# Optimization experiments

Hardware: AMD Instinct MI355X
Metric: run time of the kernel (lower is better)

## Reference

```python
import jax, jax.numpy as jnp
import numpy as np

N_NODES, N_EDGES, N_RELS, D_IN, D_OUT = 50000, 200000, 64, 32, 32


def setup_inputs() -> dict:
    key = jax.random.key(0)
    k1, k2, k3, k4, k5 = jax.random.split(key, 5)
    feat = jax.random.normal(k1, (N_NODES, D_IN), dtype=jnp.float32)
    # learned per-relation projection weights: [R, D_IN, D_OUT]
    weight = jax.random.normal(k2, (N_RELS, D_IN, D_OUT), dtype=jnp.float32) * 0.05
    src = jax.random.randint(k3, (N_EDGES,), 0, N_NODES)
    dst = jax.random.randint(k4, (N_EDGES,), 0, N_NODES)
    etypes = jax.random.randint(k5, (N_EDGES,), 0, N_RELS)
    return {"feat": feat, "weight": weight, "src": src, "dst": dst, "etypes": etypes}


def reference(feat, weight, src, dst, etypes):
    # gather source features and per-edge relation weights (HighMem variant
    # materializes W[etypes] just like torch index_select), then per-edge bmm
    n_nodes = feat.shape[0]
    msg = jnp.einsum('ei,eio->eo', feat[src], weight[etypes])  # [E, D_OUT]
    out = jax.ops.segment_sum(msg, dst, num_segments=n_nodes)  # [N, D_OUT]
    return out
```

## Files before the change

### kernel.cpp

```cpp
#include <hip/hip_runtime.h>


#define D 32
#define NRELS 64
#define BLOCK 512
#define WPB (BLOCK / 64)
#define GRID 512
#define MAXCHUNK BLOCK
#define MAXTILES (NRELS + MAXCHUNK / 16)

typedef __bf16 bf16x8 __attribute__((ext_vector_type(8)));
typedef float  f32x4  __attribute__((ext_vector_type(4)));

__global__ __launch_bounds__(BLOCK, 4) void rgcn_fused_kernel(
    const float* __restrict__ feat,
    const float* __restrict__ weight,
    const int*   __restrict__ src,
    const int*   __restrict__ dst,
    const int*   __restrict__ etypes,
    float*       __restrict__ out,
    int E, int chunk)
{
    __shared__ int cnt[NRELS];
    __shared__ int off[NRELS];
    __shared__ unsigned short list[MAXCHUNK];
    __shared__ unsigned short desc[MAXTILES];
    __shared__ int ntile_sh;

    int tid = threadIdx.x;
    int gbase = blockIdx.x * chunk;

    if (tid < NRELS) cnt[tid] = 0;
    __syncthreads();

    int my_r = -1, my_rank = 0;
    if (tid < chunk && gbase + tid < E) {
        my_r = etypes[gbase + tid];
        my_rank = atomicAdd(&cnt[my_r], 1);
    }
    __syncthreads();

    if (tid < 64) {
        int c = cnt[tid];
        int x = c;
        #pragma unroll
        for (int o = 1; o < 64; o <<= 1) {
            int y = __shfl_up(x, o, 64);
            if (tid >= o) x += y;
        }
        off[tid] = x - c;

        int nt = (c + 15) >> 4;
        int tx = nt;
        #pragma unroll
        for (int o = 1; o < 64; o <<= 1) {
            int y = __shfl_up(tx, o, 64);
            if (tid >= o) tx += y;
        }
        int tbase = tx - nt;
        for (int t = 0; t < nt; ++t)
            desc[tbase + t] = (unsigned short)((tid << 8) | t);
        if (tid == 63) ntile_sh = tx;
    }
    __syncthreads();

    if (my_r >= 0) list[off[my_r] + my_rank] = (unsigned short)tid;
    int ntiles = ntile_sh;
    __syncthreads();

    int wave = tid >> 6;
    int lane = tid & 63;
    int n    = lane & 15;
    int quad = lane >> 4;

    for (int ti = wave; ti < ntiles; ti += WPB) {
        int dsc = desc[ti];
        int r = dsc >> 8;
        int t = dsc & 255;
        int c = cnt[r];
        int mbase = t * 16;
        int mcnt = c - mbase; if (mcnt > 16) mcnt = 16;
        int lbase = off[r] + mbase;

        const float* W = weight + (size_t)r * (D * D);
        bf16x8 b0, b1;
        #pragma unroll
        for (int j = 0; j < 8; ++j) {
            int k = quad * 8 + j;
            b0[j] = (__bf16)W[k * D + n];
            b1[j] = (__bf16)W[k * D + 16 + n];
        }

        int mm = (n < mcnt) ? n : 0;
        int le = list[lbase + mm];
        int s  = src[gbase + le];
        const float4* fp = (const float4*)(feat + (size_t)s * D + quad * 8);
        float4 fa = fp[0], fb = fp[1];
        bf16x8 a;
        a[0] = (__bf16)fa.x; a[1] = (__bf16)fa.y; a[2] = (__bf16)fa.z; a[3] = (__bf16)fa.w;
        a[4] = (__bf16)fb.x; a[5] = (__bf16)fb.y; a[6] = (__bf16)fb.z; a[7] = (__bf16)fb.w;

        f32x4 z = {0.f, 0.f, 0.f, 0.f};
        f32x4 c0 = __builtin_amdgcn_mfma_f32_16x16x32_bf16(a, b0, z, 0, 0, 0);
        f32x4 c1 = __builtin_amdgcn_mfma_f32_16x16x32_bf16(a, b1, z, 0, 0, 0);

        #pragma unroll
        for (int v = 0; v < 4; ++v) {
            int m2 = quad * 4 + v;
            if (m2 < mcnt) {
                int le2 = list[lbase + m2];
                int d = dst[gbase + le2];
                atomicAdd(out + (size_t)d * D + n,      c0[v]);
                atomicAdd(out + (size_t)d * D + 16 + n, c1[v]);
            }
        }
    }
}


__global__ __launch_bounds__(256) void rgcn_edge_kernel(
    const float* __restrict__ feat, const float* __restrict__ weight,
    const int* __restrict__ src, const int* __restrict__ dst,
    const int* __restrict__ etypes, float* __restrict__ out, int n_edges)
{
    int gid = blockIdx.x * blockDim.x + threadIdx.x;
    int e = gid >> 5;
    int o = gid & 31;
    if (e >= n_edges) return;
    int s = src[e], d = dst[e], r = etypes[e];
    const float* W = weight + (size_t)r * (D * D);
    float fv = feat[(size_t)s * D + o];
    float acc = 0.f;
    #pragma unroll
    for (int i = 0; i < D; ++i) {
        float fi = __shfl(fv, i, 32);
        acc = fmaf(fi, W[i * D + o], acc);
    }
    atomicAdd(&out[(size_t)d * D + o], acc);
}

extern "C" void kernel_launch(void* const* d_in, const int* in_sizes, int n_in,
                              void* d_out, int out_size, void* d_ws, size_t ws_size,
                              hipStream_t stream) {
    const float* feat   = (const float*)d_in[0];
    const float* weight = (const float*)d_in[1];
    const int*   src    = (const int*)d_in[2];
    const int*   dst    = (const int*)d_in[3];
    const int*   etypes = (const int*)d_in[4];
    float*       out    = (float*)d_out;

    int E = in_sizes[2];

    hipMemsetAsync(d_out, 0, (size_t)out_size * sizeof(float), stream);

    int chunk = (E + GRID - 1) / GRID;
    if (chunk <= MAXCHUNK) {
        rgcn_fused_kernel<<<GRID, BLOCK, 0, stream>>>(feat, weight, src, dst,
                                                      etypes, out, E, chunk);
    } else {
        long long total = (long long)E * 32;
        int grid = (int)((total + 255) / 256);
        rgcn_edge_kernel<<<grid, 256, 0, stream>>>(feat, weight, src, dst,
                                                   etypes, out, E);
    }
}
```

Before: 97.04 us.

## Pre-convert features and weights to packed bf16 in a prep kernel, enlarge blocks

Adds a prep kernel that converts node features to bf16 and packs the relation weights into the MFMA B-operand lane layout in workspace memory. The fused kernel then loads the A and B operands as single 16-byte vectors instead of doing strided fp32 loads and per-element conversion for every tile. Blocks grow to 1024 threads with half the grid, and each wave now takes a contiguous range of tiles rather than striding through them. The cost is an extra launch plus a full pass over the feature table, and larger blocks may lower occupancy or worsen load balance across waves.

```diff
diff --git a/kernel.cpp b/kernel.cpp
--- a/kernel.cpp
+++ b/kernel.cpp
@@ -3,22 +3,63 @@
 
 #define D 32
 #define NRELS 64
-#define BLOCK 512
+#define BLOCK 1024
 #define WPB (BLOCK / 64)
-#define GRID 512
-#define MAXCHUNK BLOCK
+#define GRID 256
+#define MAXCHUNK 1024
 #define MAXTILES (NRELS + MAXCHUNK / 16)
 
 typedef __bf16 bf16x8 __attribute__((ext_vector_type(8)));
 typedef float  f32x4  __attribute__((ext_vector_type(4)));
 
+static __device__ __forceinline__ unsigned int f2b(float x) {
+    unsigned int u = __float_as_uint(x);
+    return (u + 0x7fffu + ((u >> 16) & 1u)) >> 16;
+}
+
+
+__global__ __launch_bounds__(256) void prep_kernel(
+    const float* __restrict__ feat, const float* __restrict__ weight,
+    unsigned short* __restrict__ featb,
+    unsigned short* __restrict__ wpack,
+    int n_nodes)
+{
+    int idx = blockIdx.x * 256 + threadIdx.x;
+    int nfeat = n_nodes * 4;
+    if (idx < nfeat) {
+        const float4* fp = (const float4*)(feat + (size_t)idx * 8);
+        float4 a = fp[0], b = fp[1];
+        uint4 o;
+        o.x = f2b(a.x) | (f2b(a.y) << 16);
+        o.y = f2b(a.z) | (f2b(a.w) << 16);
+        o.z = f2b(b.x) | (f2b(b.y) << 16);
+        o.w = f2b(b.z) | (f2b(b.w) << 16);
+        ((uint4*)featb)[idx] = o;
+    } else if (idx < nfeat + NRELS * 2 * 64) {
+        int t = idx - nfeat;
+        int r = t >> 7, half = (t >> 6) & 1, lane = t & 63;
+        int quad = lane >> 4, n = lane & 15;
+        const float* W = weight + (size_t)r * (D * D) + half * 16 + n;
+        uint4 o;
+        unsigned int v[8];
+        #pragma unroll
+        for (int j = 0; j < 8; ++j) v[j] = f2b(W[(quad * 8 + j) * D]);
+        o.x = v[0] | (v[1] << 16);
+        o.y = v[2] | (v[3] << 16);
+        o.z = v[4] | (v[5] << 16);
+        o.w = v[6] | (v[7] << 16);
+        ((uint4*)wpack)[t] = o;
+    }
+}
+
+
 __global__ __launch_bounds__(BLOCK, 4) void rgcn_fused_kernel(
-    const float* __restrict__ feat,
-    const float* __restrict__ weight,
-    const int*   __restrict__ src,
-    const int*   __restrict__ dst,
-    const int*   __restrict__ etypes,
-    float*       __restrict__ out,
+    const unsigned short* __restrict__ featb,
+    const unsigned short* __restrict__ wpack,
+    const int* __restrict__ src,
+    const int* __restrict__ dst,
+    const int* __restrict__ etypes,
+    float* __restrict__ out,
     int E, int chunk)
 {
     __shared__ int cnt[NRELS];
@@ -73,7 +114,11 @@
     int n    = lane & 15;
     int quad = lane >> 4;
 
-    for (int ti = wave; ti < ntiles; ti += WPB) {
+    int per = (ntiles + WPB - 1) / WPB;
+    int t0 = wave * per;
+    int t1 = t0 + per; if (t1 > ntiles) t1 = ntiles;
+
+    for (int ti = t0; ti < t1; ++ti) {
         int dsc = desc[ti];
         int r = dsc >> 8;
         int t = dsc & 255;
@@ -82,23 +127,13 @@
         int mcnt = c - mbase; if (mcnt > 16) mcnt = 16;
         int lbase = off[r] + mbase;
 
-        const float* W = weight + (size_t)r * (D * D);
-        bf16x8 b0, b1;
-        #pragma unroll
-        for (int j = 0; j < 8; ++j) {
-            int k = quad * 8 + j;
-            b0[j] = (__bf16)W[k * D + n];
-            b1[j] = (__bf16)W[k * D + 16 + n];
-        }
+        bf16x8 b0 = *(const bf16x8*)(wpack + ((size_t)(r * 2 + 0) * 64 + lane) * 8);
+        bf16x8 b1 = *(const bf16x8*)(wpack + ((size_t)(r * 2 + 1) * 64 + lane) * 8);
 
         int mm = (n < mcnt) ? n : 0;
         int le = list[lbase + mm];
         int s  = src[gbase + le];
-        const float4* fp = (const float4*)(feat + (size_t)s * D + quad * 8);
-        float4 fa = fp[0], fb = fp[1];
-        bf16x8 a;
-        a[0] = (__bf16)fa.x; a[1] = (__bf16)fa.y; a[2] = (__bf16)fa.z; a[3] = (__bf16)fa.w;
-        a[4] = (__bf16)fb.x; a[5] = (__bf16)fb.y; a[6] = (__bf16)fb.z; a[7] = (__bf16)fb.w;
+        bf16x8 a = *(const bf16x8*)(featb + (size_t)s * D + quad * 8);
 
         f32x4 z = {0.f, 0.f, 0.f, 0.f};
         f32x4 c0 = __builtin_amdgcn_mfma_f32_16x16x32_bf16(a, b0, z, 0, 0, 0);
@@ -139,6 +174,7 @@
     atomicAdd(&out[(size_t)d * D + o], acc);
 }
 
+
 extern "C" void kernel_launch(void* const* d_in, const int* in_sizes, int n_in,
                               void* d_out, int out_size, void* d_ws, size_t ws_size,
                               hipStream_t stream) {
@@ -149,18 +185,31 @@
     const int*   etypes = (const int*)d_in[4];
     float*       out    = (float*)d_out;
 
+    int N = in_sizes[0] / D;
+    int R = in_sizes[1] / (D * D);
     int E = in_sizes[2];
 
     hipMemsetAsync(d_out, 0, (size_t)out_size * sizeof(float), stream);
 
     int chunk = (E + GRID - 1) / GRID;
-    if (chunk <= MAXCHUNK) {
-        rgcn_fused_kernel<<<GRID, BLOCK, 0, stream>>>(feat, weight, src, dst,
-                                                      etypes, out, E, chunk);
-    } else {
+    size_t featb_elems = (size_t)N * D;
+    size_t need = (featb_elems + (size_t)NRELS * 2 * 64 * 8) * sizeof(unsigned short);
+
+    if (R != NRELS || chunk > MAXCHUNK || ws_size < need) {
         long long total = (long long)E * 32;
         int grid = (int)((total + 255) / 256);
         rgcn_edge_kernel<<<grid, 256, 0, stream>>>(feat, weight, src, dst,
                                                    etypes, out, E);
-    }
-}
+        return;
+    }
+
+    unsigned short* featb = (unsigned short*)d_ws;
+    unsigned short* wpack = featb + featb_elems;
+
+    int prep_tasks = N * 4 + NRELS * 2 * 64;
+    int prep_grid = (prep_tasks + 255) / 256;
+    prep_kernel<<<prep_grid, 256, 0, stream>>>(feat, weight, featb, wpack, N);
+
+    rgcn_fused_kernel<<<GRID, BLOCK, 0, stream>>>(featb, wpack, src, dst,
+                                                  etypes, out, E, chunk);
+}
```

Measured after the change: 94.99 us. 1.02x faster.
